# Kernel optimization log

Measured on AMD Instinct MI355X. Metric: run time of the kernel, lower is better.

Reference implementation:

```python
import jax, jax.numpy as jnp
import numpy as np

N_EMBD = 1024
N_HEAD = 16
T_LEN = 4096
BATCH = 1


def setup_inputs() -> dict:
    key = jax.random.key(0)
    ks = jax.random.split(key, 9)
    C = N_EMBD
    s = 1.0 / np.sqrt(C)
    inp = {
        "x": jax.random.normal(ks[0], (BATCH, T_LEN, C), dtype=jnp.float32),
        "wq": jax.random.normal(ks[1], (C, C), dtype=jnp.float32) * s,
        "bq": jax.random.normal(ks[2], (C,), dtype=jnp.float32) * s,
        "wk": jax.random.normal(ks[3], (C, C), dtype=jnp.float32) * s,
        "bk": jax.random.normal(ks[4], (C,), dtype=jnp.float32) * s,
        "wv": jax.random.normal(ks[5], (C, C), dtype=jnp.float32) * s,
        "bv": jax.random.normal(ks[6], (C,), dtype=jnp.float32) * s,
        "wp": jax.random.normal(ks[7], (C, C), dtype=jnp.float32) * s,
        "bp": jax.random.normal(ks[8], (C,), dtype=jnp.float32) * s,
    }
    return inp


def reference(x, wq, bq, wk, bk, wv, bv, wp, bp):
    B, T, C = x.shape
    H = N_HEAD
    D = C // H  # head_dim
    # torch nn.Linear: y = x @ W.T + b
    def lin(x, w, b):
        return jnp.einsum("btc,oc->bto", x, w) + b
    q = lin(x, wq, bq).reshape(B, T, H, D).transpose(0, 2, 1, 3)  # bhtd
    k = lin(x, wk, bk).reshape(B, T, H, D).transpose(0, 2, 1, 3)
    v = lin(x, wv, bv).reshape(B, T, H, D).transpose(0, 2, 1, 3)
    att = jnp.einsum("bhqd,bhkd->bhqk", q, k) / jnp.sqrt(jnp.float32(D))
    causal = jnp.tril(jnp.ones((T, T), dtype=bool))  # [T,T]
    att = jnp.where(causal[None, None, :, :], att, -jnp.inf)
    att = jax.nn.softmax(att, axis=-1)
    # dropout p=0.0 -> identity (eval equivalent)
    y = jnp.einsum("bhqk,bhkd->bhqd", att, v)
    y = y.transpose(0, 2, 1, 3).reshape(B, T, C)
    return jnp.einsum("btc,oc->bto", y, wp) + bp
```

## Files before the change

### kernel.cpp

```cpp
#include <hip/hip_runtime.h>
#include <stdint.h>

#define T_LEN 4096
#define C_DIM 1024
#define NH 16
#define LSTR 72
#define CLOG2E 0.18033688011112042f

typedef uint16_t u16;
typedef __attribute__((ext_vector_type(4))) float f32x4;
typedef __attribute__((ext_vector_type(8))) __bf16 bf16x8;
typedef __attribute__((ext_vector_type(8))) uint16_t u16x8;
typedef __attribute__((ext_vector_type(4))) uint16_t u16x4;
typedef __attribute__((ext_vector_type(4))) float fvec4;

static __device__ __forceinline__ u16 f2b(float f) {
  union { float f; uint32_t u; } v; v.f = f;
  uint32_t u = v.u;
  return (u16)((u + 0x7fffu + ((u >> 16) & 1u)) >> 16);
}

static __device__ __forceinline__ uint32_t cvtpk(float lo, float hi) {
  uint32_t r;
  asm("v_cvt_pk_bf16_f32 %0, %1, %2" : "=v"(r) : "v"(lo), "v"(hi));
  return r;
}

static __device__ __forceinline__ f32x4 mfma16(u16x8 a, u16x8 b, f32x4 c) {
  return __builtin_amdgcn_mfma_f32_16x16x32_bf16(
      __builtin_bit_cast(bf16x8, a), __builtin_bit_cast(bf16x8, b), c, 0, 0, 0);
}

static __device__ __forceinline__ void gload_lds16(const void* g, void* l) {
  __builtin_amdgcn_global_load_lds(
      (const __attribute__((address_space(1))) uint32_t*)g,
      (__attribute__((address_space(3))) uint32_t*)l, 16, 0, 0);
}

__global__ void cvt_kernel(const float* __restrict__ in, u16* __restrict__ out, int n8) {
  int i = blockIdx.x * blockDim.x + threadIdx.x;
  if (i >= n8) return;
  const fvec4* p = (const fvec4*)(in + (size_t)i * 8);
  fvec4 a = p[0], b = p[1];
  u16x8 o;
  o[0] = f2b(a[0]); o[1] = f2b(a[1]); o[2] = f2b(a[2]); o[3] = f2b(a[3]);
  o[4] = f2b(b[0]); o[5] = f2b(b[1]); o[6] = f2b(b[2]); o[7] = f2b(b[3]);
  *(u16x8*)(out + (size_t)i * 8) = o;
}

__global__ void wcvt_kernel(const float* __restrict__ w0, const float* __restrict__ w1,
                            const float* __restrict__ w2, const float* __restrict__ w3,
                            u16* __restrict__ o0, u16* __restrict__ o1,
                            u16* __restrict__ o2, u16* __restrict__ o3, int n8) {
  int i = blockIdx.x * blockDim.x + threadIdx.x;
  if (i >= n8) return;
  const int z = blockIdx.y;
  const float* in = (z == 0) ? w0 : (z == 1) ? w1 : (z == 2) ? w2 : w3;
  u16* out = (z == 0) ? o0 : (z == 1) ? o1 : (z == 2) ? o2 : o3;
  const fvec4* p = (const fvec4*)(in + (size_t)i * 8);
  fvec4 a = p[0], b = p[1];
  u16x8 o;
  o[0] = f2b(a[0]); o[1] = f2b(a[1]); o[2] = f2b(a[2]); o[3] = f2b(a[3]);
  o[4] = f2b(b[0]); o[5] = f2b(b[1]); o[6] = f2b(b[2]); o[7] = f2b(b[3]);
  *(u16x8*)(out + (size_t)i * 8) = o;
}

__global__ __launch_bounds__(256) void gemm_qkv(
    const u16* __restrict__ xb,
    const u16* __restrict__ wqb, const u16* __restrict__ wkb, const u16* __restrict__ wvb,
    const float* __restrict__ bq, const float* __restrict__ bk, const float* __restrict__ bv,
    u16* __restrict__ qh, u16* __restrict__ kh, u16* __restrict__ vt)
{
  __shared__ u16 sA[128 * 32];
  __shared__ u16 sB[128 * 32];
  const int K = C_DIM;
  const int z = blockIdx.z;
  const u16* wb = (z == 0) ? wqb : (z == 1) ? wkb : wvb;
  const float* bias = (z == 0) ? bq : (z == 1) ? bk : bv;
  const int m0 = blockIdx.x * 128;
  const int n0 = blockIdx.y * 128;
  const int tid = threadIdx.x;
  const int lane = tid & 63;
  const int w = tid >> 6;
  const int wm = (w >> 1) * 64;
  const int wn = (w & 1) * 64;
  const int lr = lane & 15;
  const int lk = (lane >> 4) * 8;

  f32x4 acc[4][4];
#pragma unroll
  for (int m = 0; m < 4; ++m)
#pragma unroll
    for (int n = 0; n < 4; ++n) acc[m][n] = (f32x4){0.f, 0.f, 0.f, 0.f};

  const int srow = tid >> 2;
  const int scol = (tid & 3) * 8;
  const u16* gA = xb + (size_t)(m0 + srow) * K + scol;
  const u16* gB = wb + (size_t)(n0 + srow) * K + scol;

  for (int k0 = 0; k0 < K; k0 += 32) {
    gload_lds16(gA + k0,          &sA[tid * 8]);
    gload_lds16(gA + 64 * K + k0, &sA[2048 + tid * 8]);
    gload_lds16(gB + k0,          &sB[tid * 8]);
    gload_lds16(gB + 64 * K + k0, &sB[2048 + tid * 8]);
    __syncthreads();
    u16x8 af[4], bfr[4];
#pragma unroll
    for (int m = 0; m < 4; ++m) af[m]  = *(const u16x8*)&sA[(wm + m * 16 + lr) * 32 + lk];
#pragma unroll
    for (int n = 0; n < 4; ++n) bfr[n] = *(const u16x8*)&sB[(wn + n * 16 + lr) * 32 + lk];
#pragma unroll
    for (int m = 0; m < 4; ++m)
#pragma unroll
      for (int n = 0; n < 4; ++n) acc[m][n] = mfma16(af[m], bfr[n], acc[m][n]);
    __syncthreads();
  }

  const int lg = lane >> 4;
#pragma unroll
  for (int n = 0; n < 4; ++n) {
    const int o = n0 + wn + n * 16 + lr;
    const float bb = bias[o];
    const int h = o >> 6;
    const int d = o & 63;
#pragma unroll
    for (int m = 0; m < 4; ++m) {
      const int tb = m0 + wm + m * 16 + lg * 4;
      if (z == 2) {
        uint2 pk;
        pk.x = cvtpk(acc[m][n][0] + bb, acc[m][n][1] + bb);
        pk.y = cvtpk(acc[m][n][2] + bb, acc[m][n][3] + bb);
        *(uint2*)&vt[(size_t)o * T_LEN + tb] = pk;
      } else if (z == 0) {
#pragma unroll
        for (int r = 0; r < 4; ++r)
          qh[((size_t)h * T_LEN + tb + r) * 64 + d] = f2b((acc[m][n][r] + bb) * CLOG2E);
      } else {
#pragma unroll
        for (int r = 0; r < 4; ++r)
          kh[((size_t)h * T_LEN + tb + r) * 64 + d] = f2b(acc[m][n][r] + bb);
      }
    }
  }
}

__global__ __launch_bounds__(256) void gemm_proj(
    const u16* __restrict__ yb, const u16* __restrict__ wpb,
    const float* __restrict__ bp, float* __restrict__ out)
{
  __shared__ u16 sA[128 * 32];
  __shared__ u16 sB[128 * 32];
  const int K = C_DIM;
  const int m0 = blockIdx.x * 128;
  const int n0 = blockIdx.y * 128;
  const int tid = threadIdx.x;
  const int lane = tid & 63;
  const int w = tid >> 6;
  const int wm = (w >> 1) * 64;
  const int wn = (w & 1) * 64;
  const int lr = lane & 15;
  const int lk = (lane >> 4) * 8;

  f32x4 acc[4][4];
#pragma unroll
  for (int m = 0; m < 4; ++m)
#pragma unroll
    for (int n = 0; n < 4; ++n) acc[m][n] = (f32x4){0.f, 0.f, 0.f, 0.f};

  const int srow = tid >> 2;
  const int scol = (tid & 3) * 8;
  const u16* gA = yb  + (size_t)(m0 + srow) * K + scol;
  const u16* gB = wpb + (size_t)(n0 + srow) * K + scol;

  for (int k0 = 0; k0 < K; k0 += 32) {
    gload_lds16(gA + k0,          &sA[tid * 8]);
    gload_lds16(gA + 64 * K + k0, &sA[2048 + tid * 8]);
    gload_lds16(gB + k0,          &sB[tid * 8]);
    gload_lds16(gB + 64 * K + k0, &sB[2048 + tid * 8]);
    __syncthreads();
    u16x8 af[4], bfr[4];
#pragma unroll
    for (int m = 0; m < 4; ++m) af[m]  = *(const u16x8*)&sA[(wm + m * 16 + lr) * 32 + lk];
#pragma unroll
    for (int n = 0; n < 4; ++n) bfr[n] = *(const u16x8*)&sB[(wn + n * 16 + lr) * 32 + lk];
#pragma unroll
    for (int m = 0; m < 4; ++m)
#pragma unroll
      for (int n = 0; n < 4; ++n) acc[m][n] = mfma16(af[m], bfr[n], acc[m][n]);
    __syncthreads();
  }

  const int lg = lane >> 4;
#pragma unroll
  for (int n = 0; n < 4; ++n) {
    const int o = n0 + wn + n * 16 + lr;
    const float bb = bp[o];
#pragma unroll
    for (int m = 0; m < 4; ++m) {
      const int tb = m0 + wm + m * 16 + lg * 4;
#pragma unroll
      for (int r = 0; r < 4; ++r)
        out[(size_t)(tb + r) * C_DIM + o] = acc[m][n][r] + bb;
    }
  }
}

__global__ __launch_bounds__(256) void attn_kernel(
    const u16* __restrict__ qh, const u16* __restrict__ kh, const u16* __restrict__ vt,
    u16* __restrict__ y)
{
  __shared__ char skb[2][8192];
  __shared__ char svb[2][8192];
  __shared__ u16 pp[4][16][LSTR];
  const int bid = blockIdx.x;
  const int j = bid >> 3;
  const int h = ((bid & 7) << 1) + (j & 1);
  const int qb = 63 - (j >> 1);
  const int nt = qb + 1;
  const int tid = threadIdx.x;
  const int lane = tid & 63;
  const int w = tid >> 6;
  const int lr = lane & 15;
  const int lg = lane >> 4;
  const int sw = (lr & 7) << 4;
  const int qt0 = qb * 64 + w * 16;

  const int srow = tid >> 2;
  const int scb = (tid & 3) * 32;
  const int wo0 = srow * 128 + (scb ^ ((srow & 7) << 4));
  const int wo1 = srow * 128 + ((scb + 16) ^ ((srow & 7) << 4));
  const u16* gkbase = kh + ((size_t)h * T_LEN + srow) * 64 + (tid & 3) * 16;
  const u16* gvbase = vt + ((size_t)h * 64 + srow) * T_LEN + (tid & 3) * 16;
  u16* ppw = &pp[w][0][0];

  const u16* qbase = qh + ((size_t)h * T_LEN + qt0 + lr) * 64 + lg * 8;
  u16x8 qf0 = *(const u16x8*)(qbase);
  u16x8 qf1 = *(const u16x8*)(qbase + 32);

  f32x4 oacc[4];
#pragma unroll
  for (int i = 0; i < 4; ++i) oacc[i] = (f32x4){0.f, 0.f, 0.f, 0.f};
  float mrow = -1e30f, lsum = 0.f;

  u16x8 ka = *(const u16x8*)(gkbase);
  u16x8 kb = *(const u16x8*)(gkbase + 8);
  u16x8 va = *(const u16x8*)(gvbase);
  u16x8 vb = *(const u16x8*)(gvbase + 8);
  *(u16x8*)(skb[0] + wo0) = ka; *(u16x8*)(skb[0] + wo1) = kb;
  *(u16x8*)(svb[0] + wo0) = va; *(u16x8*)(svb[0] + wo1) = vb;
  int cur = 0;

  for (int t = 0; t < nt; ++t) {
    __syncthreads();
    if (t + 1 < nt) {
      const size_t ko = (size_t)(t + 1) * 4096;
      ka = *(const u16x8*)(gkbase + ko);
      kb = *(const u16x8*)(gkbase + ko + 8);
      va = *(const u16x8*)(gvbase + (t + 1) * 64);
      vb = *(const u16x8*)(gvbase + (t + 1) * 64 + 8);
    }
    const char* skc = skb[cur];
    const char* svc = svb[cur];

    f32x4 sacc[4];
    __builtin_amdgcn_s_setprio(1);
#pragma unroll
    for (int i = 0; i < 4; ++i) {
      const int ro = (i * 16 + lr) * 128;
      u16x8 a0 = *(const u16x8*)(skc + ro + ((lg * 16) ^ sw));
      u16x8 a1 = *(const u16x8*)(skc + ro + ((lg * 16 + 64) ^ sw));
      f32x4 zz = (f32x4){0.f, 0.f, 0.f, 0.f};
      zz = mfma16(a0, qf0, zz);
      zz = mfma16(a1, qf1, zz);
      sacc[i] = zz;
    }
    __builtin_amdgcn_s_setprio(0);

    float pvv[4][4];
    float pm = -1e30f;
    if (t == nt - 1) {
      const int qg = qt0 + lr;
      const int kt0 = t * 64;
#pragma unroll
      for (int i = 0; i < 4; ++i) {
#pragma unroll
        for (int r = 0; r < 4; ++r) {
          const int kt = kt0 + i * 16 + lg * 4 + r;
          pvv[i][r] = (kt <= qg) ? sacc[i][r] : -1e30f;
        }
        pm = fmaxf(pm, fmaxf(fmaxf(pvv[i][0], pvv[i][1]), fmaxf(pvv[i][2], pvv[i][3])));
      }
    } else {
#pragma unroll
      for (int i = 0; i < 4; ++i) {
#pragma unroll
        for (int r = 0; r < 4; ++r) pvv[i][r] = sacc[i][r];
        pm = fmaxf(pm, fmaxf(fmaxf(pvv[i][0], pvv[i][1]), fmaxf(pvv[i][2], pvv[i][3])));
      }
    }

    if (!__all(pm <= mrow)) {
      float pmf = fmaxf(pm, __shfl_xor(pm, 16));
      pmf = fmaxf(pmf, __shfl_xor(pmf, 32));
      const float mnew = fmaxf(mrow, pmf);
      const float sc = exp2f(mrow - mnew);
      lsum *= sc;
#pragma unroll
      for (int i = 0; i < 4; ++i) oacc[i] *= sc;
      mrow = mnew;
    }

    float tsum = 0.f;
#pragma unroll
    for (int i = 0; i < 4; ++i) {
      float e0 = exp2f(pvv[i][0] - mrow);
      float e1 = exp2f(pvv[i][1] - mrow);
      float e2 = exp2f(pvv[i][2] - mrow);
      float e3 = exp2f(pvv[i][3] - mrow);
      tsum += (e0 + e1) + (e2 + e3);
      uint2 pk;
      pk.x = cvtpk(e0, e1);
      pk.y = cvtpk(e2, e3);
      *(uint2*)&ppw[lr * LSTR + i * 16 + lg * 4] = pk;
    }
    lsum += tsum;

    __builtin_amdgcn_s_setprio(1);
#pragma unroll
    for (int ks = 0; ks < 2; ++ks) {
      u16x8 pf = *(const u16x8*)&ppw[lr * LSTR + lg * 8 + ks * 32];
#pragma unroll
      for (int dblk = 0; dblk < 4; ++dblk) {
        const int ro = (dblk * 16 + lr) * 128;
        u16x8 vf = *(const u16x8*)(svc + ro + ((lg * 16 + ks * 64) ^ sw));
        oacc[dblk] = mfma16(vf, pf, oacc[dblk]);
      }
    }
    __builtin_amdgcn_s_setprio(0);

    if (t + 1 < nt) {
      char* dk = skb[cur ^ 1];
      char* dv = svb[cur ^ 1];
      *(u16x8*)(dk + wo0) = ka; *(u16x8*)(dk + wo1) = kb;
      *(u16x8*)(dv + wo0) = va; *(u16x8*)(dv + wo1) = vb;
    }
    cur ^= 1;
  }

  lsum += __shfl_xor(lsum, 16);
  lsum += __shfl_xor(lsum, 32);
  const float inv = 1.0f / lsum;
#pragma unroll
  for (int dblk = 0; dblk < 4; ++dblk) {
    uint2 pk;
    pk.x = cvtpk(oacc[dblk][0] * inv, oacc[dblk][1] * inv);
    pk.y = cvtpk(oacc[dblk][2] * inv, oacc[dblk][3] * inv);
    *(uint2*)&y[(size_t)(qt0 + lr) * C_DIM + h * 64 + dblk * 16 + lg * 4] = pk;
  }
}

extern "C" void kernel_launch(void* const* d_in, const int* in_sizes, int n_in,
                              void* d_out, int out_size, void* d_ws, size_t ws_size,
                              hipStream_t stream) {
  const float* x  = (const float*)d_in[0];
  const float* wq = (const float*)d_in[1];
  const float* bq = (const float*)d_in[2];
  const float* wk = (const float*)d_in[3];
  const float* bk = (const float*)d_in[4];
  const float* wv = (const float*)d_in[5];
  const float* bv = (const float*)d_in[6];
  const float* wp = (const float*)d_in[7];
  const float* bp = (const float*)d_in[8];

  char* ws = (char*)d_ws;
  const size_t MB = 1024 * 1024;
  u16* xb  = (u16*)(ws + 0 * MB);
  u16* wqb = (u16*)(ws + 8 * MB);
  u16* wkb = (u16*)(ws + 10 * MB);
  u16* wvb = (u16*)(ws + 12 * MB);
  u16* wpb = (u16*)(ws + 14 * MB);
  u16* qh  = (u16*)(ws + 16 * MB);
  u16* kh  = (u16*)(ws + 24 * MB);
  u16* vt  = (u16*)(ws + 32 * MB);
  u16* y   = (u16*)(ws + 40 * MB);

  cvt_kernel<<<dim3(2048), dim3(256), 0, stream>>>(x, xb, 524288);
  wcvt_kernel<<<dim3(512, 4), dim3(256), 0, stream>>>(
      wq, wk, wv, wp, wqb, wkb, wvb, wpb, 131072);

  gemm_qkv<<<dim3(32, 8, 3), dim3(256), 0, stream>>>(
      xb, wqb, wkb, wvb, bq, bk, bv, qh, kh, vt);

  attn_kernel<<<dim3(1024), dim3(256), 0, stream>>>(qh, kh, vt, y);

  gemm_proj<<<dim3(32, 8), dim3(256), 0, stream>>>(y, wpb, bp, (float*)d_out);
}
```

Before: 151.9 us.

## Process two 16-row query tiles per wave to reuse K/V tiles

Each wave now handles 32 query rows (two independent softmax states) instead of 16, so each block covers 128 queries and the grid is halved. Every K/V tile staged in LDS feeds twice as many MFMAs, reducing global and LDS traffic per query. The cost is higher register pressure, a larger P scratch buffer, and fewer blocks, which may hurt occupancy and load balance across the causal triangle.

```diff
diff --git a/kernel.cpp b/kernel.cpp
--- a/kernel.cpp
+++ b/kernel.cpp
@@ -211,19 +211,19 @@
 {
   __shared__ char skb[2][8192];
   __shared__ char svb[2][8192];
-  __shared__ u16 pp[4][16][LSTR];
+  __shared__ u16 pp[4][32][LSTR];
   const int bid = blockIdx.x;
   const int j = bid >> 3;
   const int h = ((bid & 7) << 1) + (j & 1);
-  const int qb = 63 - (j >> 1);
-  const int nt = qb + 1;
+  const int qb = 31 - (j >> 1);
+  const int nt = 2 * qb + 2;
   const int tid = threadIdx.x;
   const int lane = tid & 63;
   const int w = tid >> 6;
   const int lr = lane & 15;
   const int lg = lane >> 4;
   const int sw = (lr & 7) << 4;
-  const int qt0 = qb * 64 + w * 16;
+  const int qt0 = qb * 128 + w * 32;
 
   const int srow = tid >> 2;
   const int scb = (tid & 3) * 32;
@@ -233,14 +233,20 @@
   const u16* gvbase = vt + ((size_t)h * 64 + srow) * T_LEN + (tid & 3) * 16;
   u16* ppw = &pp[w][0][0];
 
-  const u16* qbase = qh + ((size_t)h * T_LEN + qt0 + lr) * 64 + lg * 8;
-  u16x8 qf0 = *(const u16x8*)(qbase);
-  u16x8 qf1 = *(const u16x8*)(qbase + 32);
-
-  f32x4 oacc[4];
-#pragma unroll
-  for (int i = 0; i < 4; ++i) oacc[i] = (f32x4){0.f, 0.f, 0.f, 0.f};
-  float mrow = -1e30f, lsum = 0.f;
+  const u16* qbA = qh + ((size_t)h * T_LEN + qt0 + lr) * 64 + lg * 8;
+  const u16* qbB = qbA + 16 * 64;
+  u16x8 qfA0 = *(const u16x8*)(qbA);
+  u16x8 qfA1 = *(const u16x8*)(qbA + 32);
+  u16x8 qfB0 = *(const u16x8*)(qbB);
+  u16x8 qfB1 = *(const u16x8*)(qbB + 32);
+
+  f32x4 oacc[4][2];
+#pragma unroll
+  for (int i = 0; i < 4; ++i) {
+    oacc[i][0] = (f32x4){0.f, 0.f, 0.f, 0.f};
+    oacc[i][1] = (f32x4){0.f, 0.f, 0.f, 0.f};
+  }
+  float mrowA = -1e30f, mrowB = -1e30f, lsumA = 0.f, lsumB = 0.f;
 
   u16x8 ka = *(const u16x8*)(gkbase);
   u16x8 kb = *(const u16x8*)(gkbase + 8);
@@ -262,7 +268,7 @@
     const char* skc = skb[cur];
     const char* svc = svb[cur];
 
-    f32x4 sacc[4];
+    f32x4 sA[4], sB[4];
     __builtin_amdgcn_s_setprio(1);
 #pragma unroll
     for (int i = 0; i < 4; ++i) {
@@ -270,70 +276,88 @@
       u16x8 a0 = *(const u16x8*)(skc + ro + ((lg * 16) ^ sw));
       u16x8 a1 = *(const u16x8*)(skc + ro + ((lg * 16 + 64) ^ sw));
       f32x4 zz = (f32x4){0.f, 0.f, 0.f, 0.f};
-      zz = mfma16(a0, qf0, zz);
-      zz = mfma16(a1, qf1, zz);
-      sacc[i] = zz;
+      f32x4 yy = (f32x4){0.f, 0.f, 0.f, 0.f};
+      zz = mfma16(a0, qfA0, zz); zz = mfma16(a1, qfA1, zz);
+      yy = mfma16(a0, qfB0, yy); yy = mfma16(a1, qfB1, yy);
+      sA[i] = zz; sB[i] = yy;
     }
     __builtin_amdgcn_s_setprio(0);
 
-    float pvv[4][4];
-    float pm = -1e30f;
-    if (t == nt - 1) {
-      const int qg = qt0 + lr;
+    float pvA[4][4], pvB[4][4];
+    float pmA = -1e30f, pmB = -1e30f;
+    if (t >= nt - 2) {
+      const int qgA = qt0 + lr;
+      const int qgB = qt0 + 16 + lr;
       const int kt0 = t * 64;
 #pragma unroll
       for (int i = 0; i < 4; ++i) {
 #pragma unroll
         for (int r = 0; r < 4; ++r) {
           const int kt = kt0 + i * 16 + lg * 4 + r;
-          pvv[i][r] = (kt <= qg) ? sacc[i][r] : -1e30f;
+          pvA[i][r] = (kt <= qgA) ? sA[i][r] : -1e30f;
+          pvB[i][r] = (kt <= qgB) ? sB[i][r] : -1e30f;
         }
-        pm = fmaxf(pm, fmaxf(fmaxf(pvv[i][0], pvv[i][1]), fmaxf(pvv[i][2], pvv[i][3])));
+        pmA = fmaxf(pmA, fmaxf(fmaxf(pvA[i][0], pvA[i][1]), fmaxf(pvA[i][2], pvA[i][3])));
+        pmB = fmaxf(pmB, fmaxf(fmaxf(pvB[i][0], pvB[i][1]), fmaxf(pvB[i][2], pvB[i][3])));
       }
     } else {
 #pragma unroll
       for (int i = 0; i < 4; ++i) {
 #pragma unroll
-        for (int r = 0; r < 4; ++r) pvv[i][r] = sacc[i][r];
-        pm = fmaxf(pm, fmaxf(fmaxf(pvv[i][0], pvv[i][1]), fmaxf(pvv[i][2], pvv[i][3])));
+        for (int r = 0; r < 4; ++r) { pvA[i][r] = sA[i][r]; pvB[i][r] = sB[i][r]; }
+        pmA = fmaxf(pmA, fmaxf(fmaxf(pvA[i][0], pvA[i][1]), fmaxf(pvA[i][2], pvA[i][3])));
+        pmB = fmaxf(pmB, fmaxf(fmaxf(pvB[i][0], pvB[i][1]), fmaxf(pvB[i][2], pvB[i][3])));
       }
     }
 
-    if (!__all(pm <= mrow)) {
-      float pmf = fmaxf(pm, __shfl_xor(pm, 16));
-      pmf = fmaxf(pmf, __shfl_xor(pmf, 32));
-      const float mnew = fmaxf(mrow, pmf);
-      const float sc = exp2f(mrow - mnew);
-      lsum *= sc;
-#pragma unroll
-      for (int i = 0; i < 4; ++i) oacc[i] *= sc;
-      mrow = mnew;
-    }
-
-    float tsum = 0.f;
+    if (!__all((pmA <= mrowA) && (pmB <= mrowB))) {
+      float pfA = fmaxf(pmA, __shfl_xor(pmA, 16));
+      pfA = fmaxf(pfA, __shfl_xor(pfA, 32));
+      float pfB = fmaxf(pmB, __shfl_xor(pmB, 16));
+      pfB = fmaxf(pfB, __shfl_xor(pfB, 32));
+      const float mnA = fmaxf(mrowA, pfA);
+      const float mnB = fmaxf(mrowB, pfB);
+      const float scA = exp2f(mrowA - mnA);
+      const float scB = exp2f(mrowB - mnB);
+      lsumA *= scA; lsumB *= scB;
+#pragma unroll
+      for (int i = 0; i < 4; ++i) { oacc[i][0] *= scA; oacc[i][1] *= scB; }
+      mrowA = mnA; mrowB = mnB;
+    }
+
 #pragma unroll
     for (int i = 0; i < 4; ++i) {
-      float e0 = exp2f(pvv[i][0] - mrow);
-      float e1 = exp2f(pvv[i][1] - mrow);
-      float e2 = exp2f(pvv[i][2] - mrow);
-      float e3 = exp2f(pvv[i][3] - mrow);
-      tsum += (e0 + e1) + (e2 + e3);
-      uint2 pk;
-      pk.x = cvtpk(e0, e1);
-      pk.y = cvtpk(e2, e3);
-      *(uint2*)&ppw[lr * LSTR + i * 16 + lg * 4] = pk;
-    }
-    lsum += tsum;
+      float a0 = exp2f(pvA[i][0] - mrowA);
+      float a1 = exp2f(pvA[i][1] - mrowA);
+      float a2 = exp2f(pvA[i][2] - mrowA);
+      float a3 = exp2f(pvA[i][3] - mrowA);
+      lsumA += (a0 + a1) + (a2 + a3);
+      uint2 pka;
+      pka.x = cvtpk(a0, a1);
+      pka.y = cvtpk(a2, a3);
+      *(uint2*)&ppw[(lr) * LSTR + i * 16 + lg * 4] = pka;
+      float b0 = exp2f(pvB[i][0] - mrowB);
+      float b1 = exp2f(pvB[i][1] - mrowB);
+      float b2 = exp2f(pvB[i][2] - mrowB);
+      float b3 = exp2f(pvB[i][3] - mrowB);
+      lsumB += (b0 + b1) + (b2 + b3);
+      uint2 pkb;
+      pkb.x = cvtpk(b0, b1);
+      pkb.y = cvtpk(b2, b3);
+      *(uint2*)&ppw[(16 + lr) * LSTR + i * 16 + lg * 4] = pkb;
+    }
 
     __builtin_amdgcn_s_setprio(1);
 #pragma unroll
     for (int ks = 0; ks < 2; ++ks) {
-      u16x8 pf = *(const u16x8*)&ppw[lr * LSTR + lg * 8 + ks * 32];
+      u16x8 pfA = *(const u16x8*)&ppw[(lr) * LSTR + lg * 8 + ks * 32];
+      u16x8 pfB = *(const u16x8*)&ppw[(16 + lr) * LSTR + lg * 8 + ks * 32];
 #pragma unroll
       for (int dblk = 0; dblk < 4; ++dblk) {
         const int ro = (dblk * 16 + lr) * 128;
         u16x8 vf = *(const u16x8*)(svc + ro + ((lg * 16 + ks * 64) ^ sw));
-        oacc[dblk] = mfma16(vf, pf, oacc[dblk]);
+        oacc[dblk][0] = mfma16(vf, pfA, oacc[dblk][0]);
+        oacc[dblk][1] = mfma16(vf, pfB, oacc[dblk][1]);
       }
     }
     __builtin_amdgcn_s_setprio(0);
@@ -347,15 +371,22 @@
     cur ^= 1;
   }
 
-  lsum += __shfl_xor(lsum, 16);
-  lsum += __shfl_xor(lsum, 32);
-  const float inv = 1.0f / lsum;
+  lsumA += __shfl_xor(lsumA, 16);
+  lsumA += __shfl_xor(lsumA, 32);
+  lsumB += __shfl_xor(lsumB, 16);
+  lsumB += __shfl_xor(lsumB, 32);
+  const float invA = 1.0f / lsumA;
+  const float invB = 1.0f / lsumB;
 #pragma unroll
   for (int dblk = 0; dblk < 4; ++dblk) {
-    uint2 pk;
-    pk.x = cvtpk(oacc[dblk][0] * inv, oacc[dblk][1] * inv);
-    pk.y = cvtpk(oacc[dblk][2] * inv, oacc[dblk][3] * inv);
-    *(uint2*)&y[(size_t)(qt0 + lr) * C_DIM + h * 64 + dblk * 16 + lg * 4] = pk;
+    uint2 pa;
+    pa.x = cvtpk(oacc[dblk][0][0] * invA, oacc[dblk][0][1] * invA);
+    pa.y = cvtpk(oacc[dblk][0][2] * invA, oacc[dblk][0][3] * invA);
+    *(uint2*)&y[(size_t)(qt0 + lr) * C_DIM + h * 64 + dblk * 16 + lg * 4] = pa;
+    uint2 pb;
+    pb.x = cvtpk(oacc[dblk][1][0] * invB, oacc[dblk][1][1] * invB);
+    pb.y = cvtpk(oacc[dblk][1][2] * invB, oacc[dblk][1][3] * invB);
+    *(uint2*)&y[(size_t)(qt0 + 16 + lr) * C_DIM + h * 64 + dblk * 16 + lg * 4] = pb;
   }
 }
 
@@ -391,7 +422,7 @@
   gemm_qkv<<<dim3(32, 8, 3), dim3(256), 0, stream>>>(
       xb, wqb, wkb, wvb, bq, bk, bv, qh, kh, vt);
 
-  attn_kernel<<<dim3(1024), dim3(256), 0, stream>>>(qh, kh, vt, y);
+  attn_kernel<<<dim3(512), dim3(256), 0, stream>>>(qh, kh, vt, y);
 
   gemm_proj<<<dim3(32, 8), dim3(256), 0, stream>>>(y, wpb, bp, (float*)d_out);
 }
```

New measurement: 190.7 us. +25.6%, slower.

## Use 32x32 MFMA in attention and pass P through register shuffles instead of LDS

Applied to the files above, without the earlier changes.

The attention kernel moves from 16x16x32 MFMA with four waves of 16 query rows to 32x32x16 MFMA with two waves of 32 query rows each (128 threads per block). The softmax probabilities are no longer staged through a per-wave LDS buffer. They are repacked in registers with cross-half-wave shuffles into the B-operand layout for the PV product, which removes LDS writes and reads plus the padding buffer. In exchange each block has half as many threads to load K/V tiles, so each thread issues twice the global loads. Register pressure also rises with the 16-wide accumulators.

```diff
diff --git a/kernel.cpp b/kernel.cpp
--- a/kernel.cpp
+++ b/kernel.cpp
@@ -4,14 +4,13 @@
 #define T_LEN 4096
 #define C_DIM 1024
 #define NH 16
-#define LSTR 72
 #define CLOG2E 0.18033688011112042f
 
 typedef uint16_t u16;
 typedef __attribute__((ext_vector_type(4))) float f32x4;
+typedef __attribute__((ext_vector_type(16))) float f32x16;
 typedef __attribute__((ext_vector_type(8))) __bf16 bf16x8;
 typedef __attribute__((ext_vector_type(8))) uint16_t u16x8;
-typedef __attribute__((ext_vector_type(4))) uint16_t u16x4;
 typedef __attribute__((ext_vector_type(4))) float fvec4;
 
 static __device__ __forceinline__ u16 f2b(float f) {
@@ -28,6 +27,11 @@
 
 static __device__ __forceinline__ f32x4 mfma16(u16x8 a, u16x8 b, f32x4 c) {
   return __builtin_amdgcn_mfma_f32_16x16x32_bf16(
+      __builtin_bit_cast(bf16x8, a), __builtin_bit_cast(bf16x8, b), c, 0, 0, 0);
+}
+
+static __device__ __forceinline__ f32x16 mfma32(u16x8 a, u16x8 b, f32x16 c) {
+  return __builtin_amdgcn_mfma_f32_32x32x16_bf16(
       __builtin_bit_cast(bf16x8, a), __builtin_bit_cast(bf16x8, b), c, 0, 0, 0);
 }
 
@@ -205,13 +209,12 @@
   }
 }
 
-__global__ __launch_bounds__(256) void attn_kernel(
+__global__ __launch_bounds__(128) void attn_kernel(
     const u16* __restrict__ qh, const u16* __restrict__ kh, const u16* __restrict__ vt,
     u16* __restrict__ y)
 {
   __shared__ char skb[2][8192];
   __shared__ char svb[2][8192];
-  __shared__ u16 pp[4][16][LSTR];
   const int bid = blockIdx.x;
   const int j = bid >> 3;
   const int h = ((bid & 7) << 1) + (j & 1);
@@ -219,143 +222,158 @@
   const int nt = qb + 1;
   const int tid = threadIdx.x;
   const int lane = tid & 63;
-  const int w = tid >> 6;
-  const int lr = lane & 15;
-  const int lg = lane >> 4;
-  const int sw = (lr & 7) << 4;
-  const int qt0 = qb * 64 + w * 16;
-
-  const int srow = tid >> 2;
-  const int scb = (tid & 3) * 32;
-  const int wo0 = srow * 128 + (scb ^ ((srow & 7) << 4));
-  const int wo1 = srow * 128 + ((scb + 16) ^ ((srow & 7) << 4));
-  const u16* gkbase = kh + ((size_t)h * T_LEN + srow) * 64 + (tid & 3) * 16;
-  const u16* gvbase = vt + ((size_t)h * 64 + srow) * T_LEN + (tid & 3) * 16;
-  u16* ppw = &pp[w][0][0];
-
-  const u16* qbase = qh + ((size_t)h * T_LEN + qt0 + lr) * 64 + lg * 8;
-  u16x8 qf0 = *(const u16x8*)(qbase);
-  u16x8 qf1 = *(const u16x8*)(qbase + 32);
-
-  f32x4 oacc[4];
-#pragma unroll
-  for (int i = 0; i < 4; ++i) oacc[i] = (f32x4){0.f, 0.f, 0.f, 0.f};
+  const int wv = tid >> 6;
+  const int l31 = lane & 31;
+  const int hi = lane >> 5;
+  const int swz = (lane & 7) << 4;
+  const int qrow = qb * 64 + wv * 32 + l31;
+
+  const int srow = tid >> 1;
+  const int scb = (tid & 1) * 64;
+  int wo0 = srow * 128 + ((scb +  0) ^ ((srow & 7) << 4));
+  int wo1 = srow * 128 + ((scb + 16) ^ ((srow & 7) << 4));
+  int wo2 = srow * 128 + ((scb + 32) ^ ((srow & 7) << 4));
+  int wo3 = srow * 128 + ((scb + 48) ^ ((srow & 7) << 4));
+  const u16* gk = kh + ((size_t)h * T_LEN + srow) * 64 + (tid & 1) * 32;
+  const u16* gv = vt + ((size_t)h * 64 + srow) * T_LEN + (tid & 1) * 32;
+
+  const u16* qbp = qh + ((size_t)h * T_LEN + qrow) * 64 + hi * 8;
+  u16x8 qf0 = *(const u16x8*)(qbp);
+  u16x8 qf1 = *(const u16x8*)(qbp + 16);
+  u16x8 qf2 = *(const u16x8*)(qbp + 32);
+  u16x8 qf3 = *(const u16x8*)(qbp + 48);
+
+  f32x16 oacc0 = {0.f,0.f,0.f,0.f,0.f,0.f,0.f,0.f,0.f,0.f,0.f,0.f,0.f,0.f,0.f,0.f};
+  f32x16 oacc1 = oacc0;
   float mrow = -1e30f, lsum = 0.f;
 
-  u16x8 ka = *(const u16x8*)(gkbase);
-  u16x8 kb = *(const u16x8*)(gkbase + 8);
-  u16x8 va = *(const u16x8*)(gvbase);
-  u16x8 vb = *(const u16x8*)(gvbase + 8);
-  *(u16x8*)(skb[0] + wo0) = ka; *(u16x8*)(skb[0] + wo1) = kb;
-  *(u16x8*)(svb[0] + wo0) = va; *(u16x8*)(svb[0] + wo1) = vb;
+  u16x8 kr0 = *(const u16x8*)(gk +  0), kr1 = *(const u16x8*)(gk +  8);
+  u16x8 kr2 = *(const u16x8*)(gk + 16), kr3 = *(const u16x8*)(gk + 24);
+  u16x8 vr0 = *(const u16x8*)(gv +  0), vr1 = *(const u16x8*)(gv +  8);
+  u16x8 vr2 = *(const u16x8*)(gv + 16), vr3 = *(const u16x8*)(gv + 24);
+  *(u16x8*)(skb[0] + wo0) = kr0; *(u16x8*)(skb[0] + wo1) = kr1;
+  *(u16x8*)(skb[0] + wo2) = kr2; *(u16x8*)(skb[0] + wo3) = kr3;
+  *(u16x8*)(svb[0] + wo0) = vr0; *(u16x8*)(svb[0] + wo1) = vr1;
+  *(u16x8*)(svb[0] + wo2) = vr2; *(u16x8*)(svb[0] + wo3) = vr3;
   int cur = 0;
 
   for (int t = 0; t < nt; ++t) {
     __syncthreads();
     if (t + 1 < nt) {
       const size_t ko = (size_t)(t + 1) * 4096;
-      ka = *(const u16x8*)(gkbase + ko);
-      kb = *(const u16x8*)(gkbase + ko + 8);
-      va = *(const u16x8*)(gvbase + (t + 1) * 64);
-      vb = *(const u16x8*)(gvbase + (t + 1) * 64 + 8);
+      kr0 = *(const u16x8*)(gk + ko);      kr1 = *(const u16x8*)(gk + ko + 8);
+      kr2 = *(const u16x8*)(gk + ko + 16); kr3 = *(const u16x8*)(gk + ko + 24);
+      const int vo = (t + 1) * 64;
+      vr0 = *(const u16x8*)(gv + vo);      vr1 = *(const u16x8*)(gv + vo + 8);
+      vr2 = *(const u16x8*)(gv + vo + 16); vr3 = *(const u16x8*)(gv + vo + 24);
     }
     const char* skc = skb[cur];
     const char* svc = svb[cur];
 
-    f32x4 sacc[4];
+    f32x16 s0 = {0.f,0.f,0.f,0.f,0.f,0.f,0.f,0.f,0.f,0.f,0.f,0.f,0.f,0.f,0.f,0.f};
+    f32x16 s1 = s0;
     __builtin_amdgcn_s_setprio(1);
 #pragma unroll
-    for (int i = 0; i < 4; ++i) {
-      const int ro = (i * 16 + lr) * 128;
-      u16x8 a0 = *(const u16x8*)(skc + ro + ((lg * 16) ^ sw));
-      u16x8 a1 = *(const u16x8*)(skc + ro + ((lg * 16 + 64) ^ sw));
-      f32x4 zz = (f32x4){0.f, 0.f, 0.f, 0.f};
-      zz = mfma16(a0, qf0, zz);
-      zz = mfma16(a1, qf1, zz);
-      sacc[i] = zz;
+    for (int d = 0; d < 4; ++d) {
+      const int co = (d * 32 + hi * 16) ^ swz;
+      u16x8 k0 = *(const u16x8*)(skc + l31 * 128 + co);
+      u16x8 k1 = *(const u16x8*)(skc + (32 + l31) * 128 + co);
+      u16x8 qf = (d == 0) ? qf0 : (d == 1) ? qf1 : (d == 2) ? qf2 : qf3;
+      s0 = mfma32(k0, qf, s0);
+      s1 = mfma32(k1, qf, s1);
     }
     __builtin_amdgcn_s_setprio(0);
 
-    float pvv[4][4];
+    if (t == nt - 1) {
+      const int kt0 = t * 64;
+#pragma unroll
+      for (int r = 0; r < 16; ++r) {
+        const int crow = (r & 3) + 8 * (r >> 2) + 4 * hi;
+        s0[r] = (kt0 + crow <= qrow) ? s0[r] : -1e30f;
+        s1[r] = (kt0 + 32 + crow <= qrow) ? s1[r] : -1e30f;
+      }
+    }
     float pm = -1e30f;
-    if (t == nt - 1) {
-      const int qg = qt0 + lr;
-      const int kt0 = t * 64;
-#pragma unroll
-      for (int i = 0; i < 4; ++i) {
-#pragma unroll
-        for (int r = 0; r < 4; ++r) {
-          const int kt = kt0 + i * 16 + lg * 4 + r;
-          pvv[i][r] = (kt <= qg) ? sacc[i][r] : -1e30f;
-        }
-        pm = fmaxf(pm, fmaxf(fmaxf(pvv[i][0], pvv[i][1]), fmaxf(pvv[i][2], pvv[i][3])));
-      }
-    } else {
-#pragma unroll
-      for (int i = 0; i < 4; ++i) {
-#pragma unroll
-        for (int r = 0; r < 4; ++r) pvv[i][r] = sacc[i][r];
-        pm = fmaxf(pm, fmaxf(fmaxf(pvv[i][0], pvv[i][1]), fmaxf(pvv[i][2], pvv[i][3])));
-      }
-    }
+#pragma unroll
+    for (int r = 0; r < 16; ++r) pm = fmaxf(pm, fmaxf(s0[r], s1[r]));
 
     if (!__all(pm <= mrow)) {
-      float pmf = fmaxf(pm, __shfl_xor(pm, 16));
-      pmf = fmaxf(pmf, __shfl_xor(pmf, 32));
+      float pmf = fmaxf(pm, __shfl_xor(pm, 32));
       const float mnew = fmaxf(mrow, pmf);
       const float sc = exp2f(mrow - mnew);
       lsum *= sc;
-#pragma unroll
-      for (int i = 0; i < 4; ++i) oacc[i] *= sc;
+      oacc0 *= sc;
+      oacc1 *= sc;
       mrow = mnew;
     }
 
-    float tsum = 0.f;
-#pragma unroll
-    for (int i = 0; i < 4; ++i) {
-      float e0 = exp2f(pvv[i][0] - mrow);
-      float e1 = exp2f(pvv[i][1] - mrow);
-      float e2 = exp2f(pvv[i][2] - mrow);
-      float e3 = exp2f(pvv[i][3] - mrow);
-      tsum += (e0 + e1) + (e2 + e3);
-      uint2 pk;
-      pk.x = cvtpk(e0, e1);
-      pk.y = cvtpk(e2, e3);
-      *(uint2*)&ppw[lr * LSTR + i * 16 + lg * 4] = pk;
-    }
-    lsum += tsum;
+#pragma unroll
+    for (int r = 0; r < 16; ++r) {
+      s0[r] = exp2f(s0[r] - mrow);
+      s1[r] = exp2f(s1[r] - mrow);
+      lsum += s0[r] + s1[r];
+    }
+
+    u16x8 pb[4];
+#pragma unroll
+    for (int ks = 0; ks < 4; ++ks) {
+      const int b8 = (ks & 1) * 8;
+      float e0, e1, e2, e3, e4, e5, e6, e7;
+      if (ks < 2) {
+        e0 = s0[b8+0]; e1 = s0[b8+1]; e2 = s0[b8+2]; e3 = s0[b8+3];
+        e4 = s0[b8+4]; e5 = s0[b8+5]; e6 = s0[b8+6]; e7 = s0[b8+7];
+      } else {
+        e0 = s1[b8+0]; e1 = s1[b8+1]; e2 = s1[b8+2]; e3 = s1[b8+3];
+        e4 = s1[b8+4]; e5 = s1[b8+5]; e6 = s1[b8+6]; e7 = s1[b8+7];
+      }
+      uint32_t a0 = cvtpk(e0, e1), a1 = cvtpk(e2, e3);
+      uint32_t b0 = cvtpk(e4, e5), b1 = cvtpk(e6, e7);
+      uint32_t snd0 = hi ? a0 : b0;
+      uint32_t snd1 = hi ? a1 : b1;
+      uint32_t rc0 = (uint32_t)__shfl_xor((int)snd0, 32);
+      uint32_t rc1 = (uint32_t)__shfl_xor((int)snd1, 32);
+      union { uint32_t w[4]; u16x8 v; } pu;
+      pu.w[0] = hi ? rc0 : a0;
+      pu.w[1] = hi ? rc1 : a1;
+      pu.w[2] = hi ? b0 : rc0;
+      pu.w[3] = hi ? b1 : rc1;
+      pb[ks] = pu.v;
+    }
 
     __builtin_amdgcn_s_setprio(1);
 #pragma unroll
-    for (int ks = 0; ks < 2; ++ks) {
-      u16x8 pf = *(const u16x8*)&ppw[lr * LSTR + lg * 8 + ks * 32];
-#pragma unroll
-      for (int dblk = 0; dblk < 4; ++dblk) {
-        const int ro = (dblk * 16 + lr) * 128;
-        u16x8 vf = *(const u16x8*)(svc + ro + ((lg * 16 + ks * 64) ^ sw));
-        oacc[dblk] = mfma16(vf, pf, oacc[dblk]);
-      }
+    for (int ks = 0; ks < 4; ++ks) {
+      const int co = (ks * 32 + hi * 16) ^ swz;
+      u16x8 v0 = *(const u16x8*)(svc + l31 * 128 + co);
+      u16x8 v1 = *(const u16x8*)(svc + (32 + l31) * 128 + co);
+      oacc0 = mfma32(v0, pb[ks], oacc0);
+      oacc1 = mfma32(v1, pb[ks], oacc1);
     }
     __builtin_amdgcn_s_setprio(0);
 
     if (t + 1 < nt) {
       char* dk = skb[cur ^ 1];
       char* dv = svb[cur ^ 1];
-      *(u16x8*)(dk + wo0) = ka; *(u16x8*)(dk + wo1) = kb;
-      *(u16x8*)(dv + wo0) = va; *(u16x8*)(dv + wo1) = vb;
+      *(u16x8*)(dk + wo0) = kr0; *(u16x8*)(dk + wo1) = kr1;
+      *(u16x8*)(dk + wo2) = kr2; *(u16x8*)(dk + wo3) = kr3;
+      *(u16x8*)(dv + wo0) = vr0; *(u16x8*)(dv + wo1) = vr1;
+      *(u16x8*)(dv + wo2) = vr2; *(u16x8*)(dv + wo3) = vr3;
     }
     cur ^= 1;
   }
 
-  lsum += __shfl_xor(lsum, 16);
   lsum += __shfl_xor(lsum, 32);
   const float inv = 1.0f / lsum;
-#pragma unroll
-  for (int dblk = 0; dblk < 4; ++dblk) {
-    uint2 pk;
-    pk.x = cvtpk(oacc[dblk][0] * inv, oacc[dblk][1] * inv);
-    pk.y = cvtpk(oacc[dblk][2] * inv, oacc[dblk][3] * inv);
-    *(uint2*)&y[(size_t)(qt0 + lr) * C_DIM + h * 64 + dblk * 16 + lg * 4] = pk;
+  u16* yb = y + (size_t)qrow * C_DIM + h * 64;
+#pragma unroll
+  for (int g = 0; g < 4; ++g) {
+    uint2 p0, p1;
+    p0.x = cvtpk(oacc0[4*g+0] * inv, oacc0[4*g+1] * inv);
+    p0.y = cvtpk(oacc0[4*g+2] * inv, oacc0[4*g+3] * inv);
+    *(uint2*)(yb + 8*g + 4*hi) = p0;
+    p1.x = cvtpk(oacc1[4*g+0] * inv, oacc1[4*g+1] * inv);
+    p1.y = cvtpk(oacc1[4*g+2] * inv, oacc1[4*g+3] * inv);
+    *(uint2*)(yb + 32 + 8*g + 4*hi) = p1;
   }
 }
 
@@ -391,7 +409,7 @@
   gemm_qkv<<<dim3(32, 8, 3), dim3(256), 0, stream>>>(
       xb, wqb, wkb, wvb, bq, bk, bv, qh, kh, vt);
 
-  attn_kernel<<<dim3(1024), dim3(256), 0, stream>>>(qh, kh, vt, y);
+  attn_kernel<<<dim3(1024), dim3(128), 0, stream>>>(qh, kh, vt, y);
 
   gemm_proj<<<dim3(32, 8), dim3(256), 0, stream>>>(y, wpb, bp, (float*)d_out);
 }
```

New measurement: 200.1 us. 31.8% more time.
